# Kernel tuning notes

Measured on AMD Instinct MI355X. Metric: run time of the kernel, lower is better.

Reference implementation:

```python
import jax, jax.numpy as jnp
import numpy as np

N_NODES, N_FEATS, HIDDEN, N_CLASS = 100000, 256, 128, 64
B, K0, K1, N_HIST = 1024, 25, 10, 5


def setup_inputs() -> dict:
    key = jax.random.key(0)
    ks = jax.random.split(key, 11)
    return {
        "feats": jax.random.normal(ks[0], (N_NODES, N_FEATS), dtype=jnp.float32),
        "history": jax.random.normal(ks[1], (N_NODES, HIDDEN), dtype=jnp.float32),
        "W0": jax.random.normal(ks[2], (2 * N_FEATS, HIDDEN), dtype=jnp.float32) * 0.05,
        "b0": jax.random.normal(ks[3], (HIDDEN,), dtype=jnp.float32) * 0.05,
        "W1": jax.random.normal(ks[4], (2 * HIDDEN, N_CLASS), dtype=jnp.float32) * 0.05,
        "b1": jax.random.normal(ks[5], (N_CLASS,), dtype=jnp.float32) * 0.05,
        "nodes": jax.random.randint(ks[6], (B,), 0, N_NODES, dtype=jnp.int64 if jax.config.jax_enable_x64 else jnp.int32),
        "neighs0": jax.random.randint(ks[7], (B, K0), 0, N_NODES),
        "neighs1": jax.random.randint(ks[8], (B, K1), 0, N_NODES),
        "neighs0_nb": jax.random.randint(ks[9], (B * K1, K0), 0, N_NODES),
        "h_nodes": jax.random.randint(ks[10], (B, N_HIST), 0, N_NODES),
    }


def _layer0(feats, W0, b0, h_prev, neighs):
    # h_prev: [M, 1, F]; neighs: [M, K0]
    neigh_feats = feats[neighs]                       # [M, K0, F] gather
    h = jnp.mean(neigh_feats, axis=1, keepdims=True)  # MeanAggregator -> [M, 1, F]
    h = jnp.concatenate([h_prev, h], axis=-1)         # [M, 1, 2F]
    return jax.nn.relu(h @ W0 + b0)                   # [M, 1, H]


def reference(feats, history, W0, b0, W1, b1, nodes, neighs0, neighs1, neighs0_nb, h_nodes):
    # ---- layer 0 for the seed nodes (x = feats[nodes], detached per source) ----
    x = jax.lax.stop_gradient(feats[nodes])           # torch: x.detach().clone()
    h_prev = x[:, None, :]                            # [B, 1, F]
    h1 = _layer0(feats, W0, b0, h_prev, neighs0)      # [B, 1, H]

    # ---- layer 1: recursive layer-0 embeddings of sampled neighbors ----
    nx = jax.lax.stop_gradient(feats[neighs1.reshape(-1)])[:, None, :]  # [B*K1, 1, F]
    neigh_original = _layer0(feats, W0, b0, nx, neighs0_nb)             # [B*K1, 1, H]
    neigh_original = neigh_original.reshape(B, K1, HIDDEN)

    # historical-activation trick (history lookups are detached in source)
    neigh_historical = jax.lax.stop_gradient(history[h_nodes])          # [B, 5, H]
    neigh_delta = neigh_original - jax.lax.stop_gradient(history[neighs1])
    neigh_delta = neigh_delta * (N_HIST / K1)
    neigh_feats = jnp.concatenate([neigh_delta, neigh_historical], axis=1)  # [B, K1+5, H]
    # NOTE: source also scatters history[neighs1] = neigh_original (side effect);
    # functional equivalent: history.at[neighs1].set(neigh_original), not returned here.

    h = jnp.mean(neigh_feats, axis=1, keepdims=True)                    # [B, 1, H]
    h = jnp.concatenate([h1, h], axis=-1)                               # [B, 1, 2H]
    h = jax.nn.relu(h @ W1 + b1)                                        # [B, 1, C]
    return h.squeeze(1)                                                 # [B, C]
```

## Files before the change

kernel.cpp:

```cpp
#include <hip/hip_runtime.h>

#define N_FEATS 256
#define HIDDEN  128
#define N_CLASS 64
#define BATCH   1024
#define K0      25
#define K1      10
#define N_HIST  5
#define M_TOTAL (BATCH + BATCH * K1)
#define KDIM    512

typedef unsigned short u16;
typedef short bf16x8 __attribute__((ext_vector_type(8)));
typedef float f32x4 __attribute__((ext_vector_type(4)));

static __device__ __forceinline__ u16 f2bf(float f) {
    union { float f; unsigned int i; } v;
    v.f = f;
    unsigned int x = v.i;
    x += ((x >> 16) & 1u) + 0x7FFFu;
    return (u16)(x >> 16);
}
static __device__ __forceinline__ unsigned int pack2(float lo, float hi) {
    return (unsigned int)f2bf(lo) | ((unsigned int)f2bf(hi) << 16);
}
static __device__ __forceinline__ int loadI(const void* p, long long i, int f64) {
    const char* cp = (const char*)p + (f64 ? (i << 3) : (i << 2));
    return *(const int*)cp;
}

__global__ void k_detect(const void* __restrict__ nodes, int* __restrict__ flag) {
    if (threadIdx.x == 0 && blockIdx.x == 0) {
        const int* p = (const int*)nodes;
        int f = 1;
        for (int i = 0; i < 8; ++i)
            if (p[2 * i + 1] != 0) f = 0;
        *flag = f;
    }
}

__global__ void k_transpose_w0(const float* __restrict__ W0, u16* __restrict__ W0T) {
    __shared__ u16 tile[32][33];
    int tx = threadIdx.x;
    int ty = threadIdx.y;
    int k0 = blockIdx.x * 32;
    int n0 = blockIdx.y * 32;
#pragma unroll
    for (int i = 0; i < 32; i += 8)
        tile[ty + i][tx] = f2bf(W0[(size_t)(k0 + ty + i) * HIDDEN + n0 + tx]);
    __syncthreads();
#pragma unroll
    for (int i = 0; i < 32; i += 8)
        W0T[(size_t)(n0 + ty + i) * KDIM + k0 + tx] = tile[tx][ty + i];
}

__global__ __launch_bounds__(512) void k_layer0(
        const float* __restrict__ feats,
        const void* __restrict__ nodes,
        const void* __restrict__ neighs0,
        const void* __restrict__ neighs1,
        const void* __restrict__ neighs0_nb,
        const u16* __restrict__ W0T,
        const float* __restrict__ b0,
        float* __restrict__ H,
        const int* __restrict__ flag) {
    __shared__ u16 Xs[16][KDIM + 8];
    const int f64 = *flag;
    int wv = threadIdx.x >> 6;
    int lane = threadIdx.x & 63;
    int row0 = blockIdx.x * 16;
    int d = lane * 4;

#pragma unroll
    for (int i = 0; i < 2; ++i) {
        int lr = wv * 2 + i;
        int g = row0 + lr;
        int selfIdx;
        const void* nbp;
        long long nbo;
        if (g < BATCH) {
            selfIdx = loadI(nodes, g, f64);
            nbp = neighs0; nbo = (long long)g * K0;
        } else {
            int rr = g - BATCH;
            selfIdx = loadI(neighs1, rr, f64);
            nbp = neighs0_nb; nbo = (long long)rr * K0;
        }
        int idx[K0];
#pragma unroll
        for (int k = 0; k < K0; ++k) idx[k] = loadI(nbp, nbo + k, f64);

        float4 sv = *(const float4*)(feats + (size_t)selfIdx * N_FEATS + d);
        float a0 = 0.f, a1 = 0.f, a2 = 0.f, a3 = 0.f;
#pragma unroll
        for (int k = 0; k < K0; ++k) {
            float4 v = *(const float4*)(feats + (size_t)idx[k] * N_FEATS + d);
            a0 += v.x; a1 += v.y; a2 += v.z; a3 += v.w;
        }
        const float inv = 1.0f / (float)K0;
        uint2 spk, mpk;
        spk.x = pack2(sv.x, sv.y);
        spk.y = pack2(sv.z, sv.w);
        mpk.x = pack2(a0 * inv, a1 * inv);
        mpk.y = pack2(a2 * inv, a3 * inv);
        *(uint2*)&Xs[lr][d] = spk;
        *(uint2*)&Xs[lr][N_FEATS + d] = mpk;
    }
    __syncthreads();

    int m = lane & 15;
    int q = lane >> 4;
    f32x4 acc = (f32x4){0.f, 0.f, 0.f, 0.f};
    const u16* bbase = W0T + (size_t)(wv * 16 + m) * KDIM + q * 8;
#pragma unroll
    for (int k0 = 0; k0 < KDIM; k0 += 32) {
        bf16x8 af = *(const bf16x8*)&Xs[m][k0 + q * 8];
        bf16x8 bf = *(const bf16x8*)(bbase + k0);
        acc = __builtin_amdgcn_mfma_f32_16x16x32_bf16(af, bf, acc, 0, 0, 0);
    }
    int col = wv * 16 + m;
    float bias = b0[col];
#pragma unroll
    for (int r = 0; r < 4; ++r) {
        float y = acc[r] + bias;
        y = y > 0.f ? y : 0.f;
        H[(size_t)(row0 + q * 4 + r) * HIDDEN + col] = y;
    }
}

__global__ __launch_bounds__(256) void k_final(
        const float* __restrict__ H,
        const float* __restrict__ history,
        const void* __restrict__ neighs1,
        const void* __restrict__ h_nodes,
        const float* __restrict__ W1,
        const float* __restrict__ b1,
        float* __restrict__ out,
        const int* __restrict__ flag) {
    __shared__ float hcat[2 * HIDDEN];
    __shared__ float red[256];
    const int f64 = *flag;
    const int tid = threadIdx.x;
    const int b = blockIdx.x;
    const int j = tid & 127;
    const int half = tid >> 7;

    float S = 0.f;
    if (half == 0) hcat[j] = H[(size_t)b * HIDDEN + j];
#pragma unroll
    for (int t = half * 5; t < half * 5 + 5; ++t) {
        float orig = H[(size_t)(BATCH + b * K1 + t) * HIDDEN + j];
        int n1 = loadI(neighs1, b * K1 + t, f64);
        float hist = history[(size_t)n1 * HIDDEN + j];
        S += 0.5f * (orig - hist);
    }
    if (half == 1) {
#pragma unroll
        for (int u = 0; u < N_HIST; ++u) {
            int hn = loadI(h_nodes, b * N_HIST + u, f64);
            S += history[(size_t)hn * HIDDEN + j];
        }
    }
    red[tid] = S;
    __syncthreads();
    if (half == 0)
        hcat[HIDDEN + j] = (red[j] + red[HIDDEN + j]) * (1.0f / 15.0f);
    __syncthreads();

    const int n = tid & 63;
    const int seg = tid >> 6;
    float p = 0.f;
#pragma unroll 8
    for (int i = seg * 64; i < seg * 64 + 64; ++i)
        p += hcat[i] * W1[(size_t)i * N_CLASS + n];
    red[tid] = p;
    __syncthreads();
    if (tid < 64) {
        float a = red[tid] + red[tid + 64] + red[tid + 128] + red[tid + 192]
                + b1[tid];
        a = a > 0.f ? a : 0.f;
        out[(size_t)b * N_CLASS + tid] = a;
    }
}

static __device__ __forceinline__ float loadF_m(const void* p, long long i, int fbf) {
    const char* cp = (const char*)p + (fbf ? (i << 1) : (i << 2));
    if (fbf) {
        union { unsigned int u; float f; } v;
        v.u = ((unsigned int)(*(const u16*)cp)) << 16;
        return v.f;
    }
    return *(const float*)cp;
}

__global__ __launch_bounds__(256) void k_fused(
        const void* __restrict__ feats,
        const void* __restrict__ history,
        const void* __restrict__ W0,
        const void* __restrict__ b0,
        const void* __restrict__ W1,
        const void* __restrict__ b1,
        const void* __restrict__ nodes,
        const void* __restrict__ neighs0,
        const void* __restrict__ neighs1,
        const void* __restrict__ neighs0_nb,
        const void* __restrict__ h_nodes,
        float* __restrict__ out) {
    __shared__ float W0s[32][128];
    __shared__ float Xs[11][KDIM];
    __shared__ float hcat[2 * HIDDEN];
    __shared__ float red[256];
    __shared__ int ibuf[K0 + 1];
    __shared__ int sflags[2];

    const int tid = threadIdx.x;
    const int b = blockIdx.x;

    if (tid == 0) {
        const int* ip = (const int*)nodes;
        int f = 1;
        for (int i = 0; i < 8; ++i)
            if (ip[2 * i + 1] != 0) f = 0;
        sflags[0] = f;
        const u16* qp = (const u16*)feats;
        int cnt = 0;
        for (int i = 0; i < 64; ++i) {
            int e = (qp[2 * i] >> 7) & 0xFF;
            if (e >= 90 && e <= 134) cnt++;
        }
        sflags[1] = (cnt >= 40) ? 1 : 0;
    }
    __syncthreads();
    const int f64 = sflags[0];
    const int fbf = sflags[1];

    for (int r = 0; r < 11; ++r) {
        __syncthreads();
        if (tid < K0) {
            long long nbo = (r == 0) ? ((long long)b * K0)
                                     : ((long long)(b * K1 + (r - 1)) * K0);
            const void* nbp = (r == 0) ? neighs0 : neighs0_nb;
            ibuf[tid] = loadI(nbp, nbo + tid, f64);
        } else if (tid == K0) {
            ibuf[K0] = (r == 0) ? loadI(nodes, b, f64)
                                : loadI(neighs1, b * K1 + (r - 1), f64);
        }
        __syncthreads();
        int sidx = ibuf[K0];
        Xs[r][tid] = loadF_m(feats, (long long)sidx * N_FEATS + tid, fbf);
        float s = 0.f;
#pragma unroll
        for (int k = 0; k < K0; ++k)
            s += loadF_m(feats, (long long)ibuf[k] * N_FEATS + tid, fbf);
        Xs[r][N_FEATS + tid] = s * (1.0f / (float)K0);
    }
    __syncthreads();

    const int c = tid & 127;
    const int ph = tid >> 7;
    float acc[11];
#pragma unroll
    for (int r = 0; r < 11; ++r) acc[r] = 0.f;

    for (int s = 0; s < 16; ++s) {
        __syncthreads();
#pragma unroll
        for (int i = 0; i < 16; ++i) {
            int idx = tid + 256 * i;
            int k = idx >> 7, cc = idx & 127;
            W0s[k][cc] = loadF_m(W0, (long long)(32 * s + k) * HIDDEN + cc, fbf);
        }
        __syncthreads();
        const int kb = 32 * s + 16 * ph;
#pragma unroll
        for (int r = 0; r < 11; ++r) {
            float a = 0.f;
#pragma unroll
            for (int j = 0; j < 16; ++j)
                a += Xs[r][kb + j] * W0s[16 * ph + j][c];
            acc[r] += a;
        }
    }

    float S = 0.f;
    float b0v = (tid < 128) ? loadF_m(b0, tid, fbf) : 0.f;
    for (int r = 0; r < 11; ++r) {
        __syncthreads();
        red[tid] = acc[r];
        __syncthreads();
        if (tid < 128) {
            float h = red[tid] + red[tid + 128] + b0v;
            h = h > 0.f ? h : 0.f;
            if (r == 0) {
                hcat[tid] = h;
            } else {
                int n1 = loadI(neighs1, b * K1 + (r - 1), f64);
                float hist = loadF_m(history, (long long)n1 * HIDDEN + tid, fbf);
                S += 0.5f * (h - hist);
            }
        }
    }
    if (tid < 128) {
#pragma unroll
        for (int u = 0; u < N_HIST; ++u) {
            int hn = loadI(h_nodes, b * N_HIST + u, f64);
            S += loadF_m(history, (long long)hn * HIDDEN + tid, fbf);
        }
        hcat[HIDDEN + tid] = S * (1.0f / 15.0f);
    }
    __syncthreads();

    const int n = tid & 63;
    const int seg = tid >> 6;
    float p = 0.f;
#pragma unroll 8
    for (int i = seg * 64; i < seg * 64 + 64; ++i)
        p += hcat[i] * loadF_m(W1, (long long)i * N_CLASS + n, fbf);
    red[tid] = p;
    __syncthreads();
    if (tid < 64) {
        float a = red[tid] + red[tid + 64] + red[tid + 128] + red[tid + 192]
                + loadF_m(b1, tid, fbf);
        a = a > 0.f ? a : 0.f;
        out[(long long)b * N_CLASS + tid] = a;
    }
}

extern "C" void kernel_launch(void* const* d_in, const int* in_sizes, int n_in,
                              void* d_out, int out_size, void* d_ws, size_t ws_size,
                              hipStream_t stream) {
    (void)out_size;
    const long long want[11] = {25600000, 12800000, 65536, 128, 16384, 64,
                                1024, 25600, 10240, 256000, 5120};
    const void* bp[11];
    for (int j = 0; j < 11; ++j) bp[j] = d_in[j < n_in ? j : 0];
    for (int j = 0; j < 11; ++j) {
        if (j < n_in && (long long)in_sizes[j] == want[j]) continue;
        for (int i = 0; i < n_in; ++i)
            if ((long long)in_sizes[i] == want[j]) { bp[j] = d_in[i]; break; }
    }

    const size_t WS_NEED = 131072 + 5767168 + 16;
    if (ws_size < WS_NEED) {
        k_fused<<<BATCH, 256, 0, stream>>>(
            bp[0], bp[1], bp[2], bp[3], bp[4], bp[5],
            bp[6], bp[7], bp[8], bp[9], bp[10], (float*)d_out);
        return;
    }

    char* ws = (char*)d_ws;
    u16* W0T  = (u16*)ws;
    float* H  = (float*)(ws + 131072);
    int* flag = (int*)(ws + 131072 + 5767168);

    k_detect<<<1, 1, 0, stream>>>(bp[6], flag);
    k_transpose_w0<<<dim3(16, 4), dim3(32, 8), 0, stream>>>((const float*)bp[2], W0T);
    k_layer0<<<M_TOTAL / 16, 512, 0, stream>>>(
        (const float*)bp[0], bp[6], bp[7], bp[8], bp[9], W0T,
        (const float*)bp[3], H, flag);
    k_final<<<BATCH, 256, 0, stream>>>(
        H, (const float*)bp[1], bp[8], bp[10],
        (const float*)bp[4], (const float*)bp[5], (float*)d_out, flag);
}
```

Measured before the change: 65.52 us.

## Project all node features through W0 first, then gather and average projections

Uses the linearity of mean and matmul to project every node's features once through both halves of W0 with fp16 MFMA, storing a 256-wide fp16 table. The aggregation kernel then gathers the compact projected rows instead of full 256-float feature rows and fuses layer 0, the history delta and the final layer. This cuts gather traffic, but it adds a dense streaming pass over all 100k nodes, needs a roughly 51 MB workspace, and switches from bf16 to fp16 rounding. It also folds the index-width detection into the transpose kernel.

```diff
diff --git a/kernel.cpp b/kernel.cpp
--- a/kernel.cpp
+++ b/kernel.cpp
@@ -9,9 +9,11 @@
 #define N_HIST  5
 #define M_TOTAL (BATCH + BATCH * K1)
 #define KDIM    512
+#define N_NODES 100000
 
 typedef unsigned short u16;
 typedef short bf16x8 __attribute__((ext_vector_type(8)));
+typedef _Float16 f16x8 __attribute__((ext_vector_type(8)));
 typedef float f32x4 __attribute__((ext_vector_type(4)));
 
 static __device__ __forceinline__ u16 f2bf(float f) {
@@ -23,6 +25,11 @@
 }
 static __device__ __forceinline__ unsigned int pack2(float lo, float hi) {
     return (unsigned int)f2bf(lo) | ((unsigned int)f2bf(hi) << 16);
+}
+static __device__ __forceinline__ u16 f2h(float f) {
+    union { _Float16 h; u16 u; } v;
+    v.h = (_Float16)f;
+    return v.u;
 }
 static __device__ __forceinline__ int loadI(const void* p, long long i, int f64) {
     const char* cp = (const char*)p + (f64 ? (i << 3) : (i << 2));
@@ -36,6 +43,183 @@
         for (int i = 0; i < 8; ++i)
             if (p[2 * i + 1] != 0) f = 0;
         *flag = f;
+    }
+}
+
+
+__global__ void k_transpose_w0h(const float* __restrict__ W0, u16* __restrict__ W0T2,
+                                const void* __restrict__ nodes, int* __restrict__ flag) {
+    if (threadIdx.x == 0 && threadIdx.y == 0 && blockIdx.x == 0 && blockIdx.y == 0) {
+        const int* p = (const int*)nodes;
+        int f = 1;
+        for (int i = 0; i < 8; ++i)
+            if (p[2 * i + 1] != 0) f = 0;
+        *flag = f;
+    }
+    __shared__ u16 tile[32][33];
+    int tx = threadIdx.x;
+    int ty = threadIdx.y;
+    int k0 = blockIdx.x * 32;
+    int n0 = blockIdx.y * 32;
+#pragma unroll
+    for (int i = 0; i < 32; i += 8)
+        tile[ty + i][tx] = f2h(W0[(size_t)(k0 + ty + i) * HIDDEN + n0 + tx]);
+    __syncthreads();
+    int roff = (k0 >= 256) ? 128 : 0;
+    int kk = k0 & 255;
+#pragma unroll
+    for (int i = 0; i < 32; i += 8)
+        W0T2[(size_t)(n0 + ty + i + roff) * 256 + kk + tx] = tile[tx][ty + i];
+}
+
+__global__ __launch_bounds__(512) void k_proj(
+        const float* __restrict__ feats,
+        const u16* __restrict__ W0T2,
+        u16* __restrict__ P) {
+    __shared__ u16 Xs[16][256 + 8];
+    int wv = threadIdx.x >> 6;
+    int lane = threadIdx.x & 63;
+    int r0 = blockIdx.x * 16;
+    int m = lane & 15, q = lane >> 4;
+
+    f16x8 B0[8], B1[8];
+    const u16* bb = W0T2 + (size_t)(wv * 32 + m) * 256 + q * 8;
+#pragma unroll
+    for (int kk = 0; kk < 8; ++kk) {
+        B0[kk] = *(const f16x8*)(bb + kk * 32);
+        B1[kk] = *(const f16x8*)(bb + 16 * 256 + kk * 32);
+    }
+
+#pragma unroll
+    for (int i = 0; i < 2; ++i) {
+        int lr = wv * 2 + i;
+        float4 v = *(const float4*)(feats + (size_t)(r0 + lr) * N_FEATS + lane * 4);
+        ushort4 pk;
+        pk.x = f2h(v.x); pk.y = f2h(v.y); pk.z = f2h(v.z); pk.w = f2h(v.w);
+        *(ushort4*)&Xs[lr][lane * 4] = pk;
+    }
+    __syncthreads();
+
+    f32x4 acc0 = (f32x4){0.f, 0.f, 0.f, 0.f};
+    f32x4 acc1 = (f32x4){0.f, 0.f, 0.f, 0.f};
+#pragma unroll
+    for (int kk = 0; kk < 8; ++kk) {
+        f16x8 af = *(const f16x8*)&Xs[m][kk * 32 + q * 8];
+        acc0 = __builtin_amdgcn_mfma_f32_16x16x32_f16(af, B0[kk], acc0, 0, 0, 0);
+        acc1 = __builtin_amdgcn_mfma_f32_16x16x32_f16(af, B1[kk], acc1, 0, 0, 0);
+    }
+#pragma unroll
+    for (int r = 0; r < 4; ++r) {
+        size_t row = (size_t)(r0 + q * 4 + r);
+        P[row * 256 + wv * 32 + m]      = f2h(acc0[r]);
+        P[row * 256 + wv * 32 + 16 + m] = f2h(acc1[r]);
+    }
+}
+
+__global__ __launch_bounds__(256) void k_gf(
+        const u16* __restrict__ P,
+        const float* __restrict__ history,
+        const void* __restrict__ nodes,
+        const void* __restrict__ neighs0,
+        const void* __restrict__ neighs1,
+        const void* __restrict__ neighs0_nb,
+        const void* __restrict__ h_nodes,
+        const float* __restrict__ b0,
+        const float* __restrict__ W1,
+        const float* __restrict__ b1,
+        float* __restrict__ out,
+        const int* __restrict__ flag) {
+    __shared__ float Hs[11][128];
+    __shared__ float hcat[2 * HIDDEN];
+    __shared__ float red[256];
+    const int f64 = *flag;
+    const int tid = threadIdx.x;
+    const int b = blockIdx.x;
+    const int wv = tid >> 6;
+    const int lane = tid & 63;
+    const int m = lane & 15;
+    const int grp = lane >> 4;
+
+    for (int r = wv; r < 11; r += 4) {
+        int selfIdx;
+        const void* nbp;
+        long long nbo;
+        if (r == 0) {
+            selfIdx = loadI(nodes, b, f64);
+            nbp = neighs0; nbo = (long long)b * K0;
+        } else {
+            int rr = b * K1 + (r - 1);
+            selfIdx = loadI(neighs1, rr, f64);
+            nbp = neighs0_nb; nbo = (long long)rr * K0;
+        }
+        int idx[K0];
+#pragma unroll
+        for (int k = 0; k < K0; ++k) idx[k] = loadI(nbp, nbo + k, f64);
+
+        float a[8];
+#pragma unroll
+        for (int i = 0; i < 8; ++i) a[i] = 0.f;
+#pragma unroll
+        for (int k = 0; k < 7; ++k) {
+            int k1 = 4 * k + grp;
+            if (k1 < K0) {
+                f16x8 v = *(const f16x8*)(P + (size_t)idx[k1] * 256 + 128 + m * 8);
+#pragma unroll
+                for (int i = 0; i < 8; ++i) a[i] += (float)v[i];
+            }
+        }
+#pragma unroll
+        for (int i = 0; i < 8; ++i) {
+            a[i] += __shfl_xor(a[i], 16);
+            a[i] += __shfl_xor(a[i], 32);
+        }
+        if (grp == 0) {
+            f16x8 sv = *(const f16x8*)(P + (size_t)selfIdx * 256 + m * 8);
+            const float inv = 1.0f / (float)K0;
+#pragma unroll
+            for (int i = 0; i < 8; ++i) {
+                float y = a[i] * inv + (float)sv[i] + b0[m * 8 + i];
+                Hs[r][m * 8 + i] = y > 0.f ? y : 0.f;
+            }
+        }
+    }
+    __syncthreads();
+
+    const int j = tid & 127;
+    const int half = tid >> 7;
+    float S = 0.f;
+    if (half == 0) hcat[j] = Hs[0][j];
+#pragma unroll
+    for (int t = half * 5; t < half * 5 + 5; ++t) {
+        int n1 = loadI(neighs1, b * K1 + t, f64);
+        S += 0.5f * (Hs[1 + t][j] - history[(size_t)n1 * HIDDEN + j]);
+    }
+    if (half == 1) {
+#pragma unroll
+        for (int u = 0; u < N_HIST; ++u) {
+            int hn = loadI(h_nodes, b * N_HIST + u, f64);
+            S += history[(size_t)hn * HIDDEN + j];
+        }
+    }
+    red[tid] = S;
+    __syncthreads();
+    if (half == 0)
+        hcat[HIDDEN + j] = (red[j] + red[HIDDEN + j]) * (1.0f / 15.0f);
+    __syncthreads();
+
+    const int n = tid & 63;
+    const int seg = tid >> 6;
+    float p = 0.f;
+#pragma unroll 8
+    for (int i = seg * 64; i < seg * 64 + 64; ++i)
+        p += hcat[i] * W1[(size_t)i * N_CLASS + n];
+    red[tid] = p;
+    __syncthreads();
+    if (tid < 64) {
+        float a = red[tid] + red[tid + 64] + red[tid + 128] + red[tid + 192]
+                + b1[tid];
+        a = a > 0.f ? a : 0.f;
+        out[(size_t)b * N_CLASS + tid] = a;
     }
 }
 
@@ -340,25 +524,44 @@
             if ((long long)in_sizes[i] == want[j]) { bp[j] = d_in[i]; break; }
     }
 
-    const size_t WS_NEED = 131072 + 5767168 + 16;
-    if (ws_size < WS_NEED) {
-        k_fused<<<BATCH, 256, 0, stream>>>(
-            bp[0], bp[1], bp[2], bp[3], bp[4], bp[5],
-            bp[6], bp[7], bp[8], bp[9], bp[10], (float*)d_out);
+    const size_t P_BYTES = (size_t)N_NODES * 256 * 2;
+    const size_t WS_NEW  = 131072 + P_BYTES + 16;
+    const size_t WS_OLD  = 131072 + 5767168 + 16;
+
+    if (ws_size >= WS_NEW) {
+        char* ws = (char*)d_ws;
+        u16* W0T2 = (u16*)ws;
+        u16* P    = (u16*)(ws + 131072);
+        int* flag = (int*)(ws + 131072 + P_BYTES);
+
+        k_transpose_w0h<<<dim3(16, 4), dim3(32, 8), 0, stream>>>(
+            (const float*)bp[2], W0T2, bp[6], flag);
+        k_proj<<<N_NODES / 16, 512, 0, stream>>>((const float*)bp[0], W0T2, P);
+        k_gf<<<BATCH, 256, 0, stream>>>(
+            P, (const float*)bp[1], bp[6], bp[7], bp[8], bp[9], bp[10],
+            (const float*)bp[3], (const float*)bp[4], (const float*)bp[5],
+            (float*)d_out, flag);
         return;
     }
 
-    char* ws = (char*)d_ws;
-    u16* W0T  = (u16*)ws;
-    float* H  = (float*)(ws + 131072);
-    int* flag = (int*)(ws + 131072 + 5767168);
-
-    k_detect<<<1, 1, 0, stream>>>(bp[6], flag);
-    k_transpose_w0<<<dim3(16, 4), dim3(32, 8), 0, stream>>>((const float*)bp[2], W0T);
-    k_layer0<<<M_TOTAL / 16, 512, 0, stream>>>(
-        (const float*)bp[0], bp[6], bp[7], bp[8], bp[9], W0T,
-        (const float*)bp[3], H, flag);
-    k_final<<<BATCH, 256, 0, stream>>>(
-        H, (const float*)bp[1], bp[8], bp[10],
-        (const float*)bp[4], (const float*)bp[5], (float*)d_out, flag);
-}
+    if (ws_size >= WS_OLD) {
+        char* ws = (char*)d_ws;
+        u16* W0T  = (u16*)ws;
+        float* H  = (float*)(ws + 131072);
+        int* flag = (int*)(ws + 131072 + 5767168);
+
+        k_detect<<<1, 1, 0, stream>>>(bp[6], flag);
+        k_transpose_w0<<<dim3(16, 4), dim3(32, 8), 0, stream>>>((const float*)bp[2], W0T);
+        k_layer0<<<M_TOTAL / 16, 512, 0, stream>>>(
+            (const float*)bp[0], bp[6], bp[7], bp[8], bp[9], W0T,
+            (const float*)bp[3], H, flag);
+        k_final<<<BATCH, 256, 0, stream>>>(
+            H, (const float*)bp[1], bp[8], bp[10],
+            (const float*)bp[4], (const float*)bp[5], (float*)d_out, flag);
+        return;
+    }
+
+    k_fused<<<BATCH, 256, 0, stream>>>(
+        bp[0], bp[1], bp[2], bp[3], bp[4], bp[5],
+        bp[6], bp[7], bp[8], bp[9], bp[10], (float*)d_out);
+}
```

Result: slower. 125.7 us (+91.9%).
